# Performance work log

Hardware: AMD Instinct MI355X
Metric: run time of the kernel (lower is better)

## Reference

```python
import jax, jax.numpy as jnp
import numpy as np

BETA = 1.0  # commitment loss weight (beta=1.0 in VQKD.__init__)

def l2norm(x, eps=1e-12):
    return x / jnp.maximum(jnp.linalg.norm(x, axis=-1, keepdims=True), eps)

def setup_inputs() -> dict:
    key = jax.random.key(0)
    k0, k1, k2, k3 = jax.random.split(key, 4)
    B, N, D_ENC, D_CODE, K = 8, 4096, 768, 32, 8192
    std = 0.02  # trunc_normal_(std=0.02) init of task layers
    return {
        "features": jax.random.normal(k0, (B, N, D_ENC), jnp.float32),
        "enc_w1": jax.random.normal(k1, (D_ENC, D_ENC), jnp.float32) * std,
        "enc_b1": jnp.zeros((D_ENC,), jnp.float32),
        "enc_w2": jax.random.normal(k2, (D_ENC, D_CODE), jnp.float32) * std,
        "enc_b2": jnp.zeros((D_CODE,), jnp.float32),
        "codebook": jax.random.normal(k3, (K, D_CODE), jnp.float32),
    }

def reference(features, enc_w1, enc_b1, enc_w2, enc_b2, codebook):
    # encode_task_layer: Linear -> Tanh -> Linear (run in fp32, as in the autocast-disabled block)
    z = jnp.tanh(features @ enc_w1 + enc_b1) @ enc_w2 + enc_b2          # [B, N, C]
    # NormEMAVectorQuantizer: l2-normalize tokens and (EMA-normalized) codebook
    z = l2norm(z)
    emb = l2norm(codebook)                                              # [K, C]
    # squared euclidean distances  ||z||^2 - 2 z.e + ||e||^2  -> [B, N, K]
    d = (jnp.sum(z * z, axis=-1, keepdims=True)
         - 2.0 * jnp.einsum('bnc,kc->bnk', z, emb)
         + jnp.sum(emb * emb, axis=-1))
    idx = jnp.argmin(d, axis=-1)                                        # [B, N] int32
    z_q_raw = emb[idx]                                                  # gather [B, N, C]
    loss = BETA * jnp.mean((jax.lax.stop_gradient(z_q_raw) - z) ** 2)   # commitment loss
    z_q = z + jax.lax.stop_gradient(z_q_raw - z)                        # straight-through
    return z_q, loss, idx
```

## Files before the change

kernel.cpp:

```cpp
#include <hip/hip_runtime.h>
#include <hip/hip_bf16.h>
#include <cstdint>
#include <cstddef>


namespace {
constexpr int TOKENS = 8 * 4096;
constexpr int DENC   = 768;
constexpr int DC     = 32;
constexpr int KC     = 8192;
constexpr int BM = 128, BN = 128, BK = 32;
constexpr int NSTEP = DENC / BK;
constexpr float WSCALE = 1024.0f;
constexpr float HSCALE = 512.0f;
constexpr float SSCALE = 512.0f;
constexpr int SCH = 256;
}

typedef _Float16 f16x8 __attribute__((ext_vector_type(8)));
typedef float    f32x4 __attribute__((ext_vector_type(4)));

__device__ inline void split2(float v, _Float16& h, _Float16& l) {
  h = (_Float16)v;
  l = (_Float16)(v - (float)h);
}

__device__ inline void gload_lds16(const void* g, void* l) {
  __builtin_amdgcn_global_load_lds(
      (const __attribute__((address_space(1))) void*)g,
      (__attribute__((address_space(3))) void*)l, 16, 0, 0);
}

__global__ void ksplitW(const float* __restrict__ W1,
                        _Float16* __restrict__ Wh, _Float16* __restrict__ Wl) {
  int n = blockIdx.y;
  int k = blockIdx.x * 256 + threadIdx.x;
  float w = W1[(size_t)k * DENC + n] * WSCALE;
  _Float16 h, l; split2(w, h, l);
  Wh[(size_t)n * DENC + k] = h;
  Wl[(size_t)n * DENC + k] = l;
}

__global__ void ksplitW2(const float* __restrict__ W2,
                         _Float16* __restrict__ W2h, _Float16* __restrict__ W2l) {
  int i = blockIdx.x * 256 + threadIdx.x;
  int k = i >> 5, c = i & 31;
  float w = W2[(size_t)k * DC + c] * WSCALE;
  _Float16 h, l; split2(w, h, l);
  W2h[(size_t)c * DENC + k] = h;
  W2l[(size_t)c * DENC + k] = l;
}

__global__ void knorm_codes(const float* __restrict__ cb,
                            float* __restrict__ embn, float* __restrict__ se2,
                            _Float16* __restrict__ Eh, _Float16* __restrict__ El) {
  int t = blockIdx.x * blockDim.x + threadIdx.x;
  int k = t >> 5, c = t & 31;
  float v = cb[(size_t)k * DC + c];
  float ss = v * v;
  #pragma unroll
  for (int m = 16; m >= 1; m >>= 1) ss += __shfl_xor(ss, m, 32);
  float nrm = fmaxf(sqrtf(ss), 1e-12f);
  float vn = v / nrm;
  embn[(size_t)k * DC + c] = vn;
  _Float16 h, l; split2(vn * SSCALE, h, l);
  Eh[(size_t)k * DC + c] = h;
  El[(size_t)k * DC + c] = l;
  float s2 = vn * vn;
  #pragma unroll
  for (int m = 16; m >= 1; m >>= 1) s2 += __shfl_xor(s2, m, 32);
  if (c == 0) se2[k] = s2 * (SSCALE * SSCALE);
}

__global__ __launch_bounds__(256, 3)
void kgemm1(const float* __restrict__ X,
            const _Float16* __restrict__ Wh, const _Float16* __restrict__ Wl,
            const float* __restrict__ bias1, float* __restrict__ H) {
  __shared__ __align__(16) float    As[4][BM][8];
  __shared__ __align__(16) _Float16 Bsm[2][4][BN][8];

  const int bid = blockIdx.x;
  const int xcd = bid & 7;
  const int w   = bid >> 3;
  const int n_t = w % 6;
  const int m_t = xcd * 32 + w / 6;
  const int m0 = m_t * BM, n0 = n_t * BN;

  const int t    = threadIdx.x;
  const int lane = t & 63;
  const int wv   = t >> 6;
  const int wm   = wv >> 1, wn = wv & 1;
  const int lrow = lane & 15;
  const int lgrp = lane >> 4;

  const float* xsrcA = X + (size_t)(m0 + wv * 32 + (lane >> 1)) * DENC + (lane & 1) * 4;
  const int bko_half = wv >> 1;
  const _Float16* bsrc[2] = {
    Wh + (size_t)(n0 + (wv & 1) * 64 + lane) * DENC,
    Wl + (size_t)(n0 + (wv & 1) * 64 + lane) * DENC };

  f32x4 acc[4][4];
  #pragma unroll
  for (int i = 0; i < 4; ++i)
    #pragma unroll
    for (int j = 0; j < 4; ++j) acc[i][j] = (f32x4)0.0f;

  char* AsB  = (char*)&As[0][0][0];
  char* BsB  = (char*)&Bsm[0][0][0][0];

  auto stage = [&](int s) {
    const int k0 = s * BK;
    #pragma unroll
    for (int r = 0; r < 4; ++r)
      gload_lds16(xsrcA + k0 + r * 8, AsB + r * 4096 + wv * 1024);
    #pragma unroll
    for (int r = 0; r < 4; ++r) {
      const int pl = r >> 1;
      const int ko = (r & 1) * 2 + bko_half;
      gload_lds16(bsrc[pl] + k0 + ko * 8, BsB + r * 4096 + wv * 1024);
    }
  };

  stage(0);
  for (int s = 0; s < NSTEP; ++s) {
    __syncthreads();

    f16x8 fah[4], fal[4];
    #pragma unroll
    for (int mf = 0; mf < 4; ++mf) {
      const int row = wm * 64 + mf * 16 + lrow;
      float4 u = *(const float4*)&As[lgrp][row][0];
      float4 v = *(const float4*)&As[lgrp][row][4];
      float va[8] = {u.x, u.y, u.z, u.w, v.x, v.y, v.z, v.w};
      f16x8 hh, ll;
      #pragma unroll
      for (int e = 0; e < 8; ++e) { _Float16 h, l; split2(va[e], h, l); hh[e] = h; ll[e] = l; }
      fah[mf] = hh; fal[mf] = ll;
    }

    #pragma unroll
    for (int nf = 0; nf < 4; ++nf) {
      const int col = wn * 64 + nf * 16 + lrow;
      f16x8 nbh = *(const f16x8*)&Bsm[0][lgrp][col][0];
      f16x8 nbl = *(const f16x8*)&Bsm[1][lgrp][col][0];
      #pragma unroll
      for (int mf = 0; mf < 4; ++mf) {
        acc[mf][nf] = __builtin_amdgcn_mfma_f32_16x16x32_f16(fah[mf], nbh, acc[mf][nf], 0, 0, 0);
        acc[mf][nf] = __builtin_amdgcn_mfma_f32_16x16x32_f16(fah[mf], nbl, acc[mf][nf], 0, 0, 0);
        acc[mf][nf] = __builtin_amdgcn_mfma_f32_16x16x32_f16(fal[mf], nbh, acc[mf][nf], 0, 0, 0);
      }
    }

    __syncthreads();
    if (s + 1 < NSTEP) stage(s + 1);
  }

  #pragma unroll
  for (int nf = 0; nf < 4; ++nf) {
    const int col = n0 + wn * 64 + nf * 16 + lrow;
    const float b = bias1[col];
    #pragma unroll
    for (int mf = 0; mf < 4; ++mf) {
      #pragma unroll
      for (int r = 0; r < 4; ++r) {
        const int row = m0 + wm * 64 + mf * 16 + lgrp * 4 + r;
        H[(size_t)row * DENC + col] = tanhf(acc[mf][nf][r] * (1.0f / WSCALE) + b);
      }
    }
  }
}

__global__ __launch_bounds__(128, 4)
void kgemm2(const float* __restrict__ H,
            const _Float16* __restrict__ W2h, const _Float16* __restrict__ W2l,
            const float* __restrict__ b2, float* __restrict__ zn) {
  const int t = threadIdx.x, lane = t & 63, wv = t >> 6;
  const int lrow = lane & 15, lgrp = lane >> 4;
  const int tb = blockIdx.x * 64 + wv * 32;

  const float* ap[2];
  #pragma unroll
  for (int mf = 0; mf < 2; ++mf)
    ap[mf] = H + (size_t)(tb + mf * 16 + lrow) * DENC + lgrp * 8;
  const _Float16* bh_p[2]; const _Float16* bl_p[2];
  #pragma unroll
  for (int nf = 0; nf < 2; ++nf) {
    size_t coff = (size_t)(nf * 16 + lrow) * DENC + lgrp * 8;
    bh_p[nf] = W2h + coff; bl_p[nf] = W2l + coff;
  }

  f32x4 acc[2][2];
  #pragma unroll
  for (int i = 0; i < 2; ++i)
    #pragma unroll
    for (int j = 0; j < 2; ++j) acc[i][j] = (f32x4)0.0f;

  for (int s = 0; s < DENC / 32; ++s) {
    const int koff = s * 32;
    f16x8 a_h[2], a_l[2], b_h[2], b_l[2];
    #pragma unroll
    for (int mf = 0; mf < 2; ++mf) {
      float4 u = *(const float4*)(ap[mf] + koff);
      float4 v = *(const float4*)(ap[mf] + koff + 4);
      float va[8] = {u.x,u.y,u.z,u.w, v.x,v.y,v.z,v.w};
      f16x8 hh, ll;
      #pragma unroll
      for (int e = 0; e < 8; ++e) { _Float16 h, l; split2(va[e] * HSCALE, h, l); hh[e]=h; ll[e]=l; }
      a_h[mf] = hh; a_l[mf] = ll;
    }
    #pragma unroll
    for (int nf = 0; nf < 2; ++nf) {
      b_h[nf] = *(const f16x8*)(bh_p[nf] + koff);
      b_l[nf] = *(const f16x8*)(bl_p[nf] + koff);
    }
    #pragma unroll
    for (int mf = 0; mf < 2; ++mf)
      #pragma unroll
      for (int nf = 0; nf < 2; ++nf) {
        acc[mf][nf] = __builtin_amdgcn_mfma_f32_16x16x32_f16(a_h[mf], b_h[nf], acc[mf][nf], 0, 0, 0);
        acc[mf][nf] = __builtin_amdgcn_mfma_f32_16x16x32_f16(a_h[mf], b_l[nf], acc[mf][nf], 0, 0, 0);
        acc[mf][nf] = __builtin_amdgcn_mfma_f32_16x16x32_f16(a_l[mf], b_h[nf], acc[mf][nf], 0, 0, 0);
      }
  }

  const float inv = 1.0f / (HSCALE * WSCALE);
  float bv[2];
  #pragma unroll
  for (int nf = 0; nf < 2; ++nf) bv[nf] = b2[nf * 16 + lrow];
  #pragma unroll
  for (int mf = 0; mf < 2; ++mf) {
    float z[2][4], ss[4];
    #pragma unroll
    for (int r = 0; r < 4; ++r) {
      #pragma unroll
      for (int nf = 0; nf < 2; ++nf) z[nf][r] = acc[mf][nf][r] * inv + bv[nf];
      float s2 = z[0][r] * z[0][r] + z[1][r] * z[1][r];
      #pragma unroll
      for (int m = 8; m >= 1; m >>= 1) s2 += __shfl_xor(s2, m, 16);
      ss[r] = s2;
    }
    #pragma unroll
    for (int r = 0; r < 4; ++r) {
      const int row = tb + mf * 16 + lgrp * 4 + r;
      float nrm = fmaxf(sqrtf(ss[r]), 1e-12f);
      #pragma unroll
      for (int nf = 0; nf < 2; ++nf)
        zn[(size_t)row * DC + nf * 16 + lrow] = z[nf][r] / nrm;
    }
  }
}

__device__ inline unsigned long long packkey(float d, int idx) {
  unsigned int u = __float_as_uint(d);
  u = (u & 0x80000000u) ? ~u : (u | 0x80000000u);
  return ((unsigned long long)u << 32) | (unsigned int)idx;
}

__global__ __launch_bounds__(256, 3)
void ksearch(const float* __restrict__ zn, const _Float16* __restrict__ Eh,
             const _Float16* __restrict__ El, const float* __restrict__ se2,
             unsigned long long* __restrict__ keys) {
  __shared__ __align__(16) _Float16 Bh[4][SCH][8], Bl[4][SCH][8];
  __shared__ float ce2[SCH];
  const int t = threadIdx.x, lane = t & 63, wv = t >> 6;
  const int tb  = blockIdx.x * 256 + wv * 64;
  const int cb0 = blockIdx.y * 1024;
  const int lr = lane & 15, ko = lane >> 4;

  f16x8 azh[4], azl[4];
  #pragma unroll
  for (int m = 0; m < 4; ++m) {
    const float* zp = zn + (size_t)(tb + m * 16 + lr) * DC + ko * 8;
    float4 u = *(const float4*)zp, v = *(const float4*)(zp + 4);
    float vals[8] = {u.x, u.y, u.z, u.w, v.x, v.y, v.z, v.w};
    f16x8 hh, ll;
    #pragma unroll
    for (int e = 0; e < 8; ++e) {
      _Float16 h, l; split2(vals[e] * SSCALE, h, l);
      hh[e] = h; ll[e] = l;
    }
    azh[m] = hh; azl[m] = ll;
  }

  float best[4][4]; int bi[4][4];
  #pragma unroll
  for (int m = 0; m < 4; ++m)
    #pragma unroll
    for (int r = 0; r < 4; ++r) { best[m][r] = 3.4e38f; bi[m][r] = 0; }

  f16x8 pb[8]; float pe2;

  for (int ch = 0; ch < 4; ++ch) {
    const int cb = cb0 + ch * SCH;
    #pragma unroll
    for (int it = 0; it < 8; ++it) {
      const _Float16* src = (it < 4) ? Eh : El;
      pb[it] = *(const f16x8*)&src[(size_t)(cb + t) * DC + (it & 3) * 8];
    }
    pe2 = se2[cb + t];
    __syncthreads();
    #pragma unroll
    for (int it = 0; it < 8; ++it) {
      _Float16 (*B)[SCH][8] = (it < 4) ? Bh : Bl;
      *(f16x8*)&B[it & 3][t][0] = pb[it];
    }
    ce2[t] = pe2;
    __syncthreads();

    #pragma unroll 4
    for (int f = 0; f < SCH / 16; ++f) {
      f16x8 bh = *(const f16x8*)&Bh[ko][f * 16 + lr][0];
      f16x8 bl = *(const f16x8*)&Bl[ko][f * 16 + lr][0];
      float e2v = ce2[f * 16 + lr];
      int  code = cb + f * 16 + lr;
      #pragma unroll
      for (int m = 0; m < 4; ++m) {
        f32x4 a = (f32x4)0.0f;
        a = __builtin_amdgcn_mfma_f32_16x16x32_f16(azh[m], bh, a, 0, 0, 0);
        a = __builtin_amdgcn_mfma_f32_16x16x32_f16(azh[m], bl, a, 0, 0, 0);
        a = __builtin_amdgcn_mfma_f32_16x16x32_f16(azl[m], bh, a, 0, 0, 0);
        #pragma unroll
        for (int r = 0; r < 4; ++r) {
          float d = fmaf(-2.0f, a[r], e2v);
          bool c = d < best[m][r];
          best[m][r] = c ? d : best[m][r];
          bi[m][r]   = c ? code : bi[m][r];
        }
      }
    }
  }

  #pragma unroll
  for (int m = 0; m < 4; ++m)
    #pragma unroll
    for (int r = 0; r < 4; ++r) {
      float bd = best[m][r]; int ix = bi[m][r];
      #pragma unroll
      for (int s = 1; s < 16; s <<= 1) {
        float od = __shfl_xor(bd, s);
        int   oi = __shfl_xor(ix, s);
        if (od < bd || (od == bd && oi < ix)) { bd = od; ix = oi; }
      }
      if ((lane & 15) == 0) {
        int token = tb + m * 16 + (lane >> 4) * 4 + r;
        atomicMin(&keys[token], packkey(bd, ix));
      }
    }
}

__global__ __launch_bounds__(1024)
void kfinal(const unsigned long long* __restrict__ keys,
            const float* __restrict__ zn, const float* __restrict__ embn,
            float* __restrict__ zq, float* __restrict__ loss,
            float* __restrict__ oidx) {
  __shared__ float red[32];
  int t = blockIdx.x * blockDim.x + threadIdx.x;
  int tok = t >> 5, c = t & 31;
  unsigned long long key = keys[tok];
  int idx = (int)(unsigned int)(key & 0xFFFFFFFFull);
  float q = embn[(size_t)idx * DC + c];
  float z = zn[t];
  zq[t] = z + (q - z);
  float d = q - z;
  float ss = d * d;
  #pragma unroll
  for (int m = 16; m >= 1; m >>= 1) ss += __shfl_xor(ss, m, 32);
  if (c == 0) {
    red[threadIdx.x >> 5] = ss;
    oidx[tok] = (float)idx;
  }
  __syncthreads();
  if (threadIdx.x < 32) {
    float v = red[threadIdx.x];
    #pragma unroll
    for (int m = 16; m >= 1; m >>= 1) v += __shfl_xor(v, m, 32);
    if (threadIdx.x == 0)
      atomicAdd(loss, v * (1.0f / (float)(TOKENS * DC)));
  }
}

extern "C" void kernel_launch(void* const* d_in, const int* in_sizes, int n_in,
                              void* d_out, int out_size, void* d_ws, size_t ws_size,
                              hipStream_t stream) {
  const float* X   = (const float*)d_in[0];
  const float* W1  = (const float*)d_in[1];
  const float* B1  = (const float*)d_in[2];
  const float* W2  = (const float*)d_in[3];
  const float* B2  = (const float*)d_in[4];
  const float* CB  = (const float*)d_in[5];

  float* out  = (float*)d_out;
  float* zq   = out;
  float* loss = out + (size_t)TOKENS * DC;
  float* oidx = loss + 1;

  char* ws = (char*)d_ws;
  size_t off = 0;
  float* H    = (float*)(ws + off); off += (size_t)TOKENS * DENC * 4;
  float* zn   = (float*)(ws + off); off += (size_t)TOKENS * DC * 4;
  float* embn = (float*)(ws + off); off += (size_t)KC * DC * 4;
  float* se2  = (float*)(ws + off); off += (size_t)KC * 4;
  _Float16* Eh = (_Float16*)(ws + off); off += (size_t)KC * DC * 2;
  _Float16* El = (_Float16*)(ws + off); off += (size_t)KC * DC * 2;
  unsigned long long* keys = (unsigned long long*)(ws + off);
  off += (size_t)TOKENS * 8;
  _Float16* W2h = (_Float16*)(ws + off); off += (size_t)DC * DENC * 2;
  _Float16* W2l = (_Float16*)(ws + off); off += (size_t)DC * DENC * 2;
  _Float16* W1h = (_Float16*)zn;
  _Float16* W1l = W1h + (size_t)DENC * DENC;

  hipMemsetAsync(loss, 0, sizeof(float), stream);
  hipMemsetAsync(keys, 0xFF, (size_t)TOKENS * 8, stream);

  ksplitW<<<dim3(DENC / 256, DENC), 256, 0, stream>>>(W1, W1h, W1l);
  ksplitW2<<<(DENC * DC) / 256, 256, 0, stream>>>(W2, W2h, W2l);
  knorm_codes<<<(KC * DC) / 256, 256, 0, stream>>>(CB, embn, se2, Eh, El);
  kgemm1<<<(TOKENS / BM) * (DENC / BN), 256, 0, stream>>>(X, W1h, W1l, B1, H);
  kgemm2<<<TOKENS / 64, 128, 0, stream>>>(H, W2h, W2l, B2, zn);
  ksearch<<<dim3(TOKENS / 256, KC / 1024), 256, 0, stream>>>(zn, Eh, El, se2, keys);
  kfinal<<<TOKENS * DC / 1024, 1024, 0, stream>>>(keys, zn, embn, zq, loss, oidx);
}
```

Measured before the change: 284.0 us.

## Fuse encoder GEMMs, keep tanh hidden in LDS, reduce partial projections

```diff
diff --git a/kernel.cpp b/kernel.cpp
--- a/kernel.cpp
+++ b/kernel.cpp
@@ -11,6 +11,7 @@
 constexpr int KC     = 8192;
 constexpr int BM = 128, BN = 128, BK = 32;
 constexpr int NSTEP = DENC / BK;
+constexpr int NT    = DENC / BN;
 constexpr float WSCALE = 1024.0f;
 constexpr float HSCALE = 512.0f;
 constexpr float SSCALE = 512.0f;
@@ -72,12 +73,16 @@
   if (c == 0) se2[k] = s2 * (SSCALE * SSCALE);
 }
 
-__global__ __launch_bounds__(256, 3)
-void kgemm1(const float* __restrict__ X,
+__global__ __launch_bounds__(256, 4)
+void kfused(const float* __restrict__ X,
             const _Float16* __restrict__ Wh, const _Float16* __restrict__ Wl,
-            const float* __restrict__ bias1, float* __restrict__ H) {
-  __shared__ __align__(16) float    As[4][BM][8];
-  __shared__ __align__(16) _Float16 Bsm[2][4][BN][8];
+            const float* __restrict__ bias1,
+            const _Float16* __restrict__ W2h, const _Float16* __restrict__ W2l,
+            float* __restrict__ zpart) {
+  __shared__ __align__(16) char smem[34816];
+  char*     AsB = smem;
+  _Float16* Bsm = (_Float16*)(smem + 16384);
+  float (*Hs)[68] = (float(*)[68])smem;
 
   const int bid = blockIdx.x;
   const int xcd = bid & 7;
@@ -93,11 +98,12 @@
   const int lrow = lane & 15;
   const int lgrp = lane >> 4;
 
-  const float* xsrcA = X + (size_t)(m0 + wv * 32 + (lane >> 1)) * DENC + (lane & 1) * 4;
-  const int bko_half = wv >> 1;
+  const int ae = (lane & 1) ^ ((lane >> 3) & 1);
+  const float* xsrcA = X + (size_t)(m0 + wv * 32 + (lane >> 1)) * DENC + ae * 4;
   const _Float16* bsrc[2] = {
     Wh + (size_t)(n0 + (wv & 1) * 64 + lane) * DENC,
     Wl + (size_t)(n0 + (wv & 1) * 64 + lane) * DENC };
+  const int bko_half = wv >> 1;
 
   f32x4 acc[4][4];
   #pragma unroll
@@ -105,9 +111,7 @@
     #pragma unroll
     for (int j = 0; j < 4; ++j) acc[i][j] = (f32x4)0.0f;
 
-  char* AsB  = (char*)&As[0][0][0];
-  char* BsB  = (char*)&Bsm[0][0][0][0];
-
+  char* BsB = (char*)Bsm;
   auto stage = [&](int s) {
     const int k0 = s * BK;
     #pragma unroll
@@ -129,8 +133,10 @@
     #pragma unroll
     for (int mf = 0; mf < 4; ++mf) {
       const int row = wm * 64 + mf * 16 + lrow;
-      float4 u = *(const float4*)&As[lgrp][row][0];
-      float4 v = *(const float4*)&As[lgrp][row][4];
+      const int b   = (row >> 2) & 1;
+      const char* base = AsB + lgrp * 4096 + row * 32;
+      float4 u = *(const float4*)(base + ((0 ^ b) << 4));
+      float4 v = *(const float4*)(base + ((1 ^ b) << 4));
       float va[8] = {u.x, u.y, u.z, u.w, v.x, v.y, v.z, v.w};
       f16x8 hh, ll;
       #pragma unroll
@@ -141,8 +147,8 @@
     #pragma unroll
     for (int nf = 0; nf < 4; ++nf) {
       const int col = wn * 64 + nf * 16 + lrow;
-      f16x8 nbh = *(const f16x8*)&Bsm[0][lgrp][col][0];
-      f16x8 nbl = *(const f16x8*)&Bsm[1][lgrp][col][0];
+      f16x8 nbh = *(const f16x8*)&Bsm[((0 * 4 + lgrp) * BN + col) * 8];
+      f16x8 nbl = *(const f16x8*)&Bsm[((1 * 4 + lgrp) * BN + col) * 8];
       #pragma unroll
       for (int mf = 0; mf < 4; ++mf) {
         acc[mf][nf] = __builtin_amdgcn_mfma_f32_16x16x32_f16(fah[mf], nbh, acc[mf][nf], 0, 0, 0);
@@ -155,99 +161,92 @@
     if (s + 1 < NSTEP) stage(s + 1);
   }
 
-  #pragma unroll
-  for (int nf = 0; nf < 4; ++nf) {
-    const int col = n0 + wn * 64 + nf * 16 + lrow;
-    const float b = bias1[col];
-    #pragma unroll
-    for (int mf = 0; mf < 4; ++mf) {
-      #pragma unroll
-      for (int r = 0; r < 4; ++r) {
-        const int row = m0 + wm * 64 + mf * 16 + lgrp * 4 + r;
-        H[(size_t)row * DENC + col] = tanhf(acc[mf][nf][r] * (1.0f / WSCALE) + b);
-      }
-    }
-  }
-}
-
-__global__ __launch_bounds__(128, 4)
-void kgemm2(const float* __restrict__ H,
-            const _Float16* __restrict__ W2h, const _Float16* __restrict__ W2l,
-            const float* __restrict__ b2, float* __restrict__ zn) {
-  const int t = threadIdx.x, lane = t & 63, wv = t >> 6;
-  const int lrow = lane & 15, lgrp = lane >> 4;
-  const int tb = blockIdx.x * 64 + wv * 32;
-
-  const float* ap[2];
+  {
+    float bv[4];
+    #pragma unroll
+    for (int nf = 0; nf < 4; ++nf) bv[nf] = bias1[n0 + wn * 64 + nf * 16 + lrow];
+    #pragma unroll
+    for (int mf = 0; mf < 4; ++mf)
+      #pragma unroll
+      for (int nf = 0; nf < 4; ++nf)
+        #pragma unroll
+        for (int r = 0; r < 4; ++r)
+          acc[mf][nf][r] = tanhf(acc[mf][nf][r] * (1.0f / WSCALE) + bv[nf]);
+  }
+
+  f32x4 zacc[2][2];
+  #pragma unroll
+  for (int i = 0; i < 2; ++i)
+    #pragma unroll
+    for (int j = 0; j < 2; ++j) zacc[i][j] = (f32x4)0.0f;
+
+  #pragma unroll
+  for (int h = 0; h < 2; ++h) {
+    __syncthreads();
+    if (wn == h) {
+      #pragma unroll
+      for (int mf = 0; mf < 4; ++mf)
+        #pragma unroll
+        for (int nf = 0; nf < 4; ++nf)
+          #pragma unroll
+          for (int r = 0; r < 4; ++r)
+            Hs[wm * 64 + mf * 16 + lgrp * 4 + r][nf * 16 + lrow] = acc[mf][nf][r];
+    }
+    __syncthreads();
+    #pragma unroll
+    for (int ks = 0; ks < 2; ++ks) {
+      const int koct = ks * 4 + lgrp;
+      f16x8 bfh[2], bfl[2];
+      #pragma unroll
+      for (int nf = 0; nf < 2; ++nf) {
+        const int c = nf * 16 + lrow;
+        const size_t kg = (size_t)c * DENC + n0 + h * 64 + koct * 8;
+        bfh[nf] = *(const f16x8*)&W2h[kg];
+        bfl[nf] = *(const f16x8*)&W2l[kg];
+      }
+      #pragma unroll
+      for (int mf = 0; mf < 2; ++mf) {
+        const float* hp = &Hs[wv * 32 + mf * 16 + lrow][koct * 8];
+        float4 u = *(const float4*)hp, v = *(const float4*)(hp + 4);
+        float va[8] = {u.x, u.y, u.z, u.w, v.x, v.y, v.z, v.w};
+        f16x8 hh, ll;
+        #pragma unroll
+        for (int e = 0; e < 8; ++e) { _Float16 hx, lx; split2(va[e] * HSCALE, hx, lx); hh[e] = hx; ll[e] = lx; }
+        #pragma unroll
+        for (int nf = 0; nf < 2; ++nf) {
+          zacc[mf][nf] = __builtin_amdgcn_mfma_f32_16x16x32_f16(hh, bfh[nf], zacc[mf][nf], 0, 0, 0);
+          zacc[mf][nf] = __builtin_amdgcn_mfma_f32_16x16x32_f16(hh, bfl[nf], zacc[mf][nf], 0, 0, 0);
+          zacc[mf][nf] = __builtin_amdgcn_mfma_f32_16x16x32_f16(ll, bfh[nf], zacc[mf][nf], 0, 0, 0);
+        }
+      }
+    }
+  }
+
+  float* zp = zpart + (size_t)n_t * TOKENS * DC;
   #pragma unroll
   for (int mf = 0; mf < 2; ++mf)
-    ap[mf] = H + (size_t)(tb + mf * 16 + lrow) * DENC + lgrp * 8;
-  const _Float16* bh_p[2]; const _Float16* bl_p[2];
-  #pragma unroll
-  for (int nf = 0; nf < 2; ++nf) {
-    size_t coff = (size_t)(nf * 16 + lrow) * DENC + lgrp * 8;
-    bh_p[nf] = W2h + coff; bl_p[nf] = W2l + coff;
-  }
-
-  f32x4 acc[2][2];
-  #pragma unroll
-  for (int i = 0; i < 2; ++i)
-    #pragma unroll
-    for (int j = 0; j < 2; ++j) acc[i][j] = (f32x4)0.0f;
-
-  for (int s = 0; s < DENC / 32; ++s) {
-    const int koff = s * 32;
-    f16x8 a_h[2], a_l[2], b_h[2], b_l[2];
-    #pragma unroll
-    for (int mf = 0; mf < 2; ++mf) {
-      float4 u = *(const float4*)(ap[mf] + koff);
-      float4 v = *(const float4*)(ap[mf] + koff + 4);
-      float va[8] = {u.x,u.y,u.z,u.w, v.x,v.y,v.z,v.w};
-      f16x8 hh, ll;
-      #pragma unroll
-      for (int e = 0; e < 8; ++e) { _Float16 h, l; split2(va[e] * HSCALE, h, l); hh[e]=h; ll[e]=l; }
-      a_h[mf] = hh; a_l[mf] = ll;
-    }
-    #pragma unroll
-    for (int nf = 0; nf < 2; ++nf) {
-      b_h[nf] = *(const f16x8*)(bh_p[nf] + koff);
-      b_l[nf] = *(const f16x8*)(bl_p[nf] + koff);
-    }
-    #pragma unroll
-    for (int mf = 0; mf < 2; ++mf)
-      #pragma unroll
-      for (int nf = 0; nf < 2; ++nf) {
-        acc[mf][nf] = __builtin_amdgcn_mfma_f32_16x16x32_f16(a_h[mf], b_h[nf], acc[mf][nf], 0, 0, 0);
-        acc[mf][nf] = __builtin_amdgcn_mfma_f32_16x16x32_f16(a_h[mf], b_l[nf], acc[mf][nf], 0, 0, 0);
-        acc[mf][nf] = __builtin_amdgcn_mfma_f32_16x16x32_f16(a_l[mf], b_h[nf], acc[mf][nf], 0, 0, 0);
-      }
-  }
-
-  const float inv = 1.0f / (HSCALE * WSCALE);
-  float bv[2];
-  #pragma unroll
-  for (int nf = 0; nf < 2; ++nf) bv[nf] = b2[nf * 16 + lrow];
-  #pragma unroll
-  for (int mf = 0; mf < 2; ++mf) {
-    float z[2][4], ss[4];
     #pragma unroll
     for (int r = 0; r < 4; ++r) {
-      #pragma unroll
-      for (int nf = 0; nf < 2; ++nf) z[nf][r] = acc[mf][nf][r] * inv + bv[nf];
-      float s2 = z[0][r] * z[0][r] + z[1][r] * z[1][r];
-      #pragma unroll
-      for (int m = 8; m >= 1; m >>= 1) s2 += __shfl_xor(s2, m, 16);
-      ss[r] = s2;
-    }
-    #pragma unroll
-    for (int r = 0; r < 4; ++r) {
-      const int row = tb + mf * 16 + lgrp * 4 + r;
-      float nrm = fmaxf(sqrtf(ss[r]), 1e-12f);
+      const int row = m0 + wv * 32 + mf * 16 + lgrp * 4 + r;
       #pragma unroll
       for (int nf = 0; nf < 2; ++nf)
-        zn[(size_t)row * DC + nf * 16 + lrow] = z[nf][r] / nrm;
-    }
-  }
+        zp[(size_t)row * DC + nf * 16 + lrow] = zacc[mf][nf][r];
+    }
+}
+
+__global__ void kreduce(const float* __restrict__ zpart, const float* __restrict__ b2,
+                        float* __restrict__ zn) {
+  int t = blockIdx.x * blockDim.x + threadIdx.x;
+  int c = t & 31;
+  float s = 0.0f;
+  #pragma unroll
+  for (int nt = 0; nt < NT; ++nt) s += zpart[(size_t)nt * TOKENS * DC + t];
+  float z = s * (1.0f / (HSCALE * WSCALE)) + b2[c];
+  float ss = z * z;
+  #pragma unroll
+  for (int m = 16; m >= 1; m >>= 1) ss += __shfl_xor(ss, m, 32);
+  float nrm = fmaxf(sqrtf(ss), 1e-12f);
+  zn[t] = z / nrm;
 }
 
 __device__ inline unsigned long long packkey(float d, int idx) {
@@ -256,7 +255,7 @@
   return ((unsigned long long)u << 32) | (unsigned int)idx;
 }
 
-__global__ __launch_bounds__(256, 3)
+__global__ __launch_bounds__(256, 4)
 void ksearch(const float* __restrict__ zn, const _Float16* __restrict__ Eh,
              const _Float16* __restrict__ El, const float* __restrict__ se2,
              unsigned long long* __restrict__ keys) {
@@ -396,7 +395,7 @@
 
   char* ws = (char*)d_ws;
   size_t off = 0;
-  float* H    = (float*)(ws + off); off += (size_t)TOKENS * DENC * 4;
+  float* zpart = (float*)(ws + off); off += (size_t)NT * TOKENS * DC * 4;
   float* zn   = (float*)(ws + off); off += (size_t)TOKENS * DC * 4;
   float* embn = (float*)(ws + off); off += (size_t)KC * DC * 4;
   float* se2  = (float*)(ws + off); off += (size_t)KC * 4;
@@ -415,8 +414,8 @@
   ksplitW<<<dim3(DENC / 256, DENC), 256, 0, stream>>>(W1, W1h, W1l);
   ksplitW2<<<(DENC * DC) / 256, 256, 0, stream>>>(W2, W2h, W2l);
   knorm_codes<<<(KC * DC) / 256, 256, 0, stream>>>(CB, embn, se2, Eh, El);
-  kgemm1<<<(TOKENS / BM) * (DENC / BN), 256, 0, stream>>>(X, W1h, W1l, B1, H);
-  kgemm2<<<TOKENS / 64, 128, 0, stream>>>(H, W2h, W2l, B2, zn);
+  kfused<<<(TOKENS / BM) * (DENC / BN), 256, 0, stream>>>(X, W1h, W1l, B1, W2h, W2l, zpart);
+  kreduce<<<TOKENS * DC / 256, 256, 0, stream>>>(zpart, B2, zn);
   ksearch<<<dim3(TOKENS / 256, KC / 1024), 256, 0, stream>>>(zn, Eh, El, se2, keys);
   kfinal<<<TOKENS * DC / 1024, 1024, 0, stream>>>(keys, zn, embn, zq, loss, oidx);
 }
```

After: 262.9 us. 1.08x faster.
